# Optimization experiments

Measured on AMD Instinct MI355X. Metric: run time of the kernel, lower is better.

Reference implementation:

```python
import jax, jax.numpy as jnp
import numpy as np

G = 8       # groups
C = 64      # channels per group
KH = KW = 3 # kernel size
K = KH * KW
PAD = 1     # padding (stride=1, dilation=1)


def setup_inputs() -> dict:
    key = jax.random.key(0)
    k1, k2, k3 = jax.random.split(key, 3)
    B, H, W = 1, 100, 160
    x = jax.random.normal(k1, (B, H, W, G * C), dtype=jnp.float32)
    offset = jax.random.normal(k2, (B, H, W, G * K * 2), dtype=jnp.float32)
    mask = jax.random.normal(k3, (B, H, W, G * K), dtype=jnp.float32)
    return {"x": x, "offset": offset, "mask": mask}


def _dcn_core(x, offset, mask):
    B, H, W, _ = x.shape
    xg = x.reshape(B, H, W, G, C)
    off = offset.reshape(B, H, W, G, K, 2)
    m = jax.nn.softmax(mask.reshape(B, H, W, G, K), axis=-1)

    # kernel reference points relative to output pixel (stride=1, pad=1, dil=1)
    ky, kx = jnp.meshgrid(jnp.arange(KH, dtype=jnp.float32) - PAD,
                          jnp.arange(KW, dtype=jnp.float32) - PAD,
                          indexing="ij")
    ky = ky.reshape(K)  # [K]
    kx = kx.reshape(K)

    hh = jnp.arange(H, dtype=jnp.float32)[None, :, None, None, None]  # [1,H,1,1,1]
    ww = jnp.arange(W, dtype=jnp.float32)[None, None, :, None, None]  # [1,1,W,1,1]
    # sampling locations [B,H,W,G,K]
    loc_h = hh + ky[None, None, None, None, :] + off[..., 0]
    loc_w = ww + kx[None, None, None, None, :] + off[..., 1]

    h0 = jnp.floor(loc_h)
    w0 = jnp.floor(loc_w)
    th = loc_h - h0  # fractional parts
    tw = loc_w - w0
    h0 = h0.astype(jnp.int32)
    w0 = w0.astype(jnp.int32)

    b_idx = jnp.arange(B)[:, None, None, None, None]
    g_idx = jnp.arange(G)[None, None, None, :, None]

    def corner(hi, wi, wgt):
        valid = ((hi >= 0) & (hi < H) & (wi >= 0) & (wi < W)).astype(x.dtype)
        hi = jnp.clip(hi, 0, H - 1)
        wi = jnp.clip(wi, 0, W - 1)
        s = xg[b_idx, hi, wi, g_idx]            # [B,H,W,G,K,C]
        return s * (wgt * valid)[..., None]

    val = corner(h0,     w0,     (1 - th) * (1 - tw))
    val = val + corner(h0,     w0 + 1, (1 - th) * tw)
    val = val + corner(h0 + 1, w0,     th * (1 - tw))
    val = val + corner(h0 + 1, w0 + 1, th * tw)

    out = jnp.einsum("bhwgkc,bhwgk->bhwgc", val, m)  # modulated accumulate over K
    return out.reshape(B, H, W, G * C)


def reference(x, offset, mask):
    return _dcn_core(x, offset, mask)
```

## Files before the change

### kernel.cpp

```cpp
#include <hip/hip_runtime.h>
#include <hip/hip_fp16.h>

#define G_ 8
#define C_ 64
#define K_ 9
#define H_ 100
#define W_ 160
#define TW_ 8
#define TH_ 8
#define HALO_ 4
#define SW_ 16
#define SH_ 16
#define PLANE_ 273
#define TAB_ (8 * PLANE_)
#define NLDS_ (TAB_ + 576)

__global__ __launch_bounds__(512, 6) void dcn_kernel(
    const float* __restrict__ x,
    const float* __restrict__ offset,
    const float* __restrict__ mask,
    float* __restrict__ out)
{
    __shared__ uint4 sm[NLDS_];
    const int bid = (int)blockIdx.x;
    const int g   = bid & 7;
    const int t   = bid >> 3;
    const int th  = t / 20, twc = t % 20;
    const int h0  = th * TH_, w0 = twc * TW_;
    const int tid = (int)threadIdx.x;

#pragma unroll
    for (int it = 0; it < 4; ++it) {
        const int task = it * 512 + tid;
        const int rec  = task >> 3;
        const int c    = task & 7;
        const int i = rec >> 4, j = rec & 15;
        const int hs = min(max(h0 - HALO_ + i, 0), H_ - 1);
        const int ws = min(max(w0 - HALO_ + j, 0), W_ - 1);
        const float* src = x + (size_t)(hs * W_ + ws) * (G_ * C_) + g * C_ + c * 8;
        const float4 A = *(const float4*)src;
        const float4 B = *(const float4*)(src + 4);
        __half2 p0 = __floats2half2_rn(A.x, A.y);
        __half2 p1 = __floats2half2_rn(A.z, A.w);
        __half2 p2 = __floats2half2_rn(B.x, B.y);
        __half2 p3 = __floats2half2_rn(B.z, B.w);
        uint4 v;
        v.x = *(unsigned*)&p0; v.y = *(unsigned*)&p1;
        v.z = *(unsigned*)&p2; v.w = *(unsigned*)&p3;
        sm[c * PLANE_ + i * 17 + j] = v;
    }

    for (int task = tid; task < 576; task += 512) {
        const int px = task / 9;
        const int k  = task - px * 9;
        const int hh = h0 + (px >> 3), ww = w0 + (px & 7);
        uint4 r; r.x = 0u; r.y = 0u; r.z = 0u; r.w = 0u;
        if (hh < H_) {
            const int pixg = (hh * W_ + ww) * G_ + g;
            const float* mptr = mask + (size_t)pixg * K_;
            float mmax = -1e30f;
#pragma unroll
            for (int kk = 0; kk < K_; ++kk) mmax = fmaxf(mmax, mptr[kk]);
            float msum = 0.f;
#pragma unroll
            for (int kk = 0; kk < K_; ++kk) msum += __expf(mptr[kk] - mmax);
            const float m = __expf(mptr[k] - mmax) / msum;

            const float2 o2 = *(const float2*)(offset + (size_t)pixg * (2 * K_) + 2 * k);
            const float lh = (float)(hh + k / 3 - 1) + o2.x;
            const float lw = (float)(ww + k % 3 - 1) + o2.y;
            const float fh0 = floorf(lh), fw0 = floorf(lw);
            const float ft = lh - fh0, gt = lw - fw0;
            const int hI = (int)fh0, wI = (int)fw0;

            const float wh0 = (hI >= 0  && hI < H_    ) ? (1.f - ft) * m : 0.f;
            const float wh1 = (hI >= -1 && hI < H_ - 1) ? ft * m         : 0.f;
            const float cw0 = (wI >= 0  && wI < W_    ) ? (1.f - gt)     : 0.f;
            const float cw1 = (wI >= -1 && wI < W_ - 1) ? gt             : 0.f;
            __half2 wa = __floats2half2_rn(wh0 * cw0, wh0 * cw1);
            __half2 wb = __floats2half2_rn(wh1 * cw0, wh1 * cw1);

            const int hc0 = min(max(hI,     0), H_ - 1);
            const int hc1 = min(max(hI + 1, 0), H_ - 1);
            const int wc0 = min(max(wI,     0), W_ - 1);
            const int wc1 = min(max(wI + 1, 0), W_ - 1);

            const bool inbox = (hI >= h0 - HALO_) && (hI <= h0 + TH_ + HALO_ - 2) &&
                               (wI >= w0 - HALO_) && (wI <= w0 + TW_ + HALO_ - 2);
            if (inbox) {
                const int ri0 = hc0 - (h0 - HALO_);
                const int rj0 = wc0 - (w0 - HALO_);
                r.x = *(unsigned*)&wa;
                r.y = *(unsigned*)&wb;
                r.z = (unsigned)ri0 | ((unsigned)rj0 << 8)
                    | ((unsigned)(wc1 - wc0) << 16) | ((unsigned)(hc1 - hc0) << 17);
            } else {
                const int ri0 = min(max(hc0 - (h0 - HALO_), 0), SH_ - 1);
                const int rj0 = min(max(wc0 - (w0 - HALO_), 0), SW_ - 1);
                r.z = (unsigned)ri0 | ((unsigned)rj0 << 8) | 0x80000000u;
            }
        }
        sm[TAB_ + task] = r;
    }
    __syncthreads();

    const int px = tid >> 3;
    const int c  = tid & 7;
    const int hh = h0 + (px >> 3), ww = w0 + (px & 7);
    if (hh >= H_) return;
    const int pixg = (hh * W_ + ww) * G_ + g;
    const int pb = c * PLANE_;

    const uint4 t0 = sm[TAB_ + px * 9 + 0];
    const uint4 t1 = sm[TAB_ + px * 9 + 1];
    const uint4 t2 = sm[TAB_ + px * 9 + 2];
    const uint4 t3 = sm[TAB_ + px * 9 + 3];
    const uint4 t4 = sm[TAB_ + px * 9 + 4];
    const uint4 t5 = sm[TAB_ + px * 9 + 5];
    const uint4 t6 = sm[TAB_ + px * 9 + 6];
    const uint4 t7 = sm[TAB_ + px * 9 + 7];
    const uint4 t8 = sm[TAB_ + px * 9 + 8];

    __half2 acc[3][4];
#pragma unroll
    for (int gr = 0; gr < 3; ++gr)
#pragma unroll
        for (int u = 0; u < 4; ++u) acc[gr][u] = __half2(__half(0.f), __half(0.f));

#define FMA4(V, WD, GR)                                                       \
    {                                                                         \
        const __half2 wt_ = *(const __half2*)&(WD);                           \
        acc[GR][0] = __hfma2(*(const __half2*)&(V).x, wt_, acc[GR][0]);       \
        acc[GR][1] = __hfma2(*(const __half2*)&(V).y, wt_, acc[GR][1]);       \
        acc[GR][2] = __hfma2(*(const __half2*)&(V).z, wt_, acc[GR][2]);       \
        acc[GR][3] = __hfma2(*(const __half2*)&(V).w, wt_, acc[GR][3]);       \
    }

#define GC(GR, HC, WC, WF)                                                    \
    {                                                                         \
        const __half2 wt_ = __float2half2_rn(WF);                             \
        const float* s_ = x + (size_t)((HC) * W_ + (WC)) * (G_ * C_) + g * C_ + c * 8; \
        const float4 v0 = *(const float4*)s_;                                 \
        const float4 v1 = *(const float4*)(s_ + 4);                           \
        __half2 e0 = __floats2half2_rn(v0.x, v0.y), e1 = __floats2half2_rn(v0.z, v0.w); \
        __half2 e2 = __floats2half2_rn(v1.x, v1.y), e3 = __floats2half2_rn(v1.z, v1.w); \
        acc[GR][0] = __hfma2(e0, wt_, acc[GR][0]);                            \
        acc[GR][1] = __hfma2(e1, wt_, acc[GR][1]);                            \
        acc[GR][2] = __hfma2(e2, wt_, acc[GR][2]);                            \
        acc[GR][3] = __hfma2(e3, wt_, acc[GR][3]);                            \
    }

#define SLOWTAP(KK)                                                           \
    {                                                                         \
        const float* mptr_ = mask + (size_t)pixg * K_;                        \
        float mmax_ = -1e30f;                                                 \
        _Pragma("unroll")                                                     \
        for (int kk = 0; kk < K_; ++kk) mmax_ = fmaxf(mmax_, mptr_[kk]);      \
        float msum_ = 0.f;                                                    \
        _Pragma("unroll")                                                     \
        for (int kk = 0; kk < K_; ++kk) msum_ += __expf(mptr_[kk] - mmax_);   \
        const float m_ = __expf(mptr_[KK] - mmax_) / msum_;                   \
        const float2 o2_ = *(const float2*)(offset + (size_t)pixg * (2 * K_) + 2 * (KK)); \
        const float lh_ = (float)(hh + (KK) / 3 - 1) + o2_.x;                 \
        const float lw_ = (float)(ww + (KK) % 3 - 1) + o2_.y;                 \
        const float fh_ = floorf(lh_), fw_ = floorf(lw_);                     \
        const float ft_ = lh_ - fh_, gt_ = lw_ - fw_;                         \
        const int hI_ = (int)fh_, wI_ = (int)fw_;                             \
        const float wh0_ = (hI_ >= 0  && hI_ < H_    ) ? (1.f - ft_) * m_ : 0.f; \
        const float wh1_ = (hI_ >= -1 && hI_ < H_ - 1) ? ft_ * m_         : 0.f; \
        const float cw0_ = (wI_ >= 0  && wI_ < W_    ) ? (1.f - gt_)     : 0.f; \
        const float cw1_ = (wI_ >= -1 && wI_ < W_ - 1) ? gt_             : 0.f; \
        const int hc0_ = min(max(hI_,     0), H_ - 1);                        \
        const int hc1_ = min(max(hI_ + 1, 0), H_ - 1);                        \
        const int wc0_ = min(max(wI_,     0), W_ - 1);                        \
        const int wc1_ = min(max(wI_ + 1, 0), W_ - 1);                        \
        GC((KK) / 3, hc0_, wc0_, wh0_ * cw0_)                                 \
        GC((KK) / 3, hc0_, wc1_, wh0_ * cw1_)                                 \
        GC((KK) / 3, hc1_, wc0_, wh1_ * cw0_)                                 \
        GC((KK) / 3, hc1_, wc1_, wh1_ * cw1_)                                 \
    }

#define TAP(KK, R)                                                            \
    {                                                                         \
        const int ri0_ = (int)((R).z & 0xffu);                                \
        const int rj0_ = (int)(((R).z >> 8) & 0xffu);                         \
        const int dc_  = (int)(((R).z >> 16) & 1u);                           \
        const int dr17_ = (((R).z >> 17) & 1u) ? 17 : 0;                      \
        const int i00_ = pb + ri0_ * 17 + rj0_;                               \
        const int i01_ = i00_ + dc_;                                          \
        const int i10_ = i00_ + dr17_;                                        \
        const int i11_ = i10_ + dc_;                                          \
        const unsigned W00d = __builtin_amdgcn_perm((R).x, (R).x, 0x01000100u); \
        const unsigned W01d = __builtin_amdgcn_perm((R).x, (R).x, 0x03020302u); \
        const unsigned W10d = __builtin_amdgcn_perm((R).y, (R).y, 0x01000100u); \
        const unsigned W11d = __builtin_amdgcn_perm((R).y, (R).y, 0x03020302u); \
        const uint4 vA_ = sm[i00_];                                           \
        const uint4 vB_ = sm[i01_];                                           \
        const uint4 vC_ = sm[i10_];                                           \
        const uint4 vD_ = sm[i11_];                                           \
        FMA4(vA_, W00d, (KK) / 3)                                             \
        FMA4(vB_, W01d, (KK) / 3)                                             \
        FMA4(vC_, W10d, (KK) / 3)                                             \
        FMA4(vD_, W11d, (KK) / 3)                                             \
        if (__builtin_expect(((R).z >> 31) != 0u, 0)) { SLOWTAP(KK) }         \
    }

    TAP(0, t0) TAP(1, t1) TAP(2, t2)
    TAP(3, t3) TAP(4, t4) TAP(5, t5)
    TAP(6, t6) TAP(7, t7) TAP(8, t8)

#undef TAP
#undef SLOWTAP
#undef GC
#undef FMA4

    float* op = out + (size_t)pixg * C_ + c * 8;
    {
        const float2 s0 = __half22float2(acc[0][0]);
        const float2 a0 = __half22float2(acc[1][0]);
        const float2 b0 = __half22float2(acc[2][0]);
        const float2 s1 = __half22float2(acc[0][1]);
        const float2 a1 = __half22float2(acc[1][1]);
        const float2 b1 = __half22float2(acc[2][1]);
        const float2 s2 = __half22float2(acc[0][2]);
        const float2 a2 = __half22float2(acc[1][2]);
        const float2 b2 = __half22float2(acc[2][2]);
        const float2 s3 = __half22float2(acc[0][3]);
        const float2 a3 = __half22float2(acc[1][3]);
        const float2 b3 = __half22float2(acc[2][3]);
        float4 o1, o2;
        o1.x = s0.x + a0.x + b0.x;  o1.y = s0.y + a0.y + b0.y;
        o1.z = s1.x + a1.x + b1.x;  o1.w = s1.y + a1.y + b1.y;
        o2.x = s2.x + a2.x + b2.x;  o2.y = s2.y + a2.y + b2.y;
        o2.z = s3.x + a3.x + b3.x;  o2.w = s3.y + a3.y + b3.y;
        *(float4*)op       = o1;
        *(float4*)(op + 4) = o2;
    }
}

extern "C" void kernel_launch(void* const* d_in, const int* in_sizes, int n_in,
                              void* d_out, int out_size, void* d_ws, size_t ws_size,
                              hipStream_t stream) {
    const float* x      = (const float*)d_in[0];
    const float* offset = (const float*)d_in[1];
    const float* mask   = (const float*)d_in[2];
    float* out          = (float*)d_out;

    dcn_kernel<<<2080, 512, 0, stream>>>(x, offset, mask, out);
}
```

Measured before the change: 30.30 us.

## Swizzle LDS tile layout, split tap table into SoA arrays, raise occupancy

Replaces the padded-row (stride 17) LDS layout for the fp16 input halo with a 16-wide row layout using an XOR swizzle on the column index, shrinking LDS per plane. The per-tap table moves from a uint4 array, which carried an unused word, to three separate unsigned arrays loaded lazily inside each tap rather than all up front. Launch bounds rise from 6 to 8 blocks per CU to exploit the smaller LDS footprint and lower register pressure. The swizzle adds index arithmetic per corner and may change bank-conflict patterns for the gather reads.

```diff
diff --git a/kernel.cpp b/kernel.cpp
--- a/kernel.cpp
+++ b/kernel.cpp
@@ -11,17 +11,18 @@
 #define HALO_ 4
 #define SW_ 16
 #define SH_ 16
-#define PLANE_ 273
-#define TAB_ (8 * PLANE_)
-#define NLDS_ (TAB_ + 576)
-
-__global__ __launch_bounds__(512, 6) void dcn_kernel(
+#define PLANE_ 257
+#define NXP_ (8 * PLANE_)
+
+__global__ __launch_bounds__(512, 8) void dcn_kernel(
     const float* __restrict__ x,
     const float* __restrict__ offset,
     const float* __restrict__ mask,
     float* __restrict__ out)
 {
-    __shared__ uint4 sm[NLDS_];
+    __shared__ uint4 smx[NXP_];
+    __shared__ unsigned smw0[576], smw1[576], smidx[576];
+
     const int bid = (int)blockIdx.x;
     const int g   = bid & 7;
     const int t   = bid >> 3;
@@ -47,14 +48,14 @@
         uint4 v;
         v.x = *(unsigned*)&p0; v.y = *(unsigned*)&p1;
         v.z = *(unsigned*)&p2; v.w = *(unsigned*)&p3;
-        sm[c * PLANE_ + i * 17 + j] = v;
+        smx[c * PLANE_ + i * 16 + (j ^ (i & 7))] = v;
     }
 
     for (int task = tid; task < 576; task += 512) {
         const int px = task / 9;
         const int k  = task - px * 9;
         const int hh = h0 + (px >> 3), ww = w0 + (px & 7);
-        uint4 r; r.x = 0u; r.y = 0u; r.z = 0u; r.w = 0u;
+        unsigned rw0 = 0u, rw1 = 0u, ridx = 0u;
         if (hh < H_) {
             const int pixg = (hh * W_ + ww) * G_ + g;
             const float* mptr = mask + (size_t)pixg * K_;
@@ -90,17 +91,19 @@
             if (inbox) {
                 const int ri0 = hc0 - (h0 - HALO_);
                 const int rj0 = wc0 - (w0 - HALO_);
-                r.x = *(unsigned*)&wa;
-                r.y = *(unsigned*)&wb;
-                r.z = (unsigned)ri0 | ((unsigned)rj0 << 8)
-                    | ((unsigned)(wc1 - wc0) << 16) | ((unsigned)(hc1 - hc0) << 17);
+                rw0 = *(unsigned*)&wa;
+                rw1 = *(unsigned*)&wb;
+                ridx = (unsigned)ri0 | ((unsigned)rj0 << 8)
+                     | ((unsigned)(wc1 - wc0) << 16) | ((unsigned)(hc1 - hc0) << 17);
             } else {
                 const int ri0 = min(max(hc0 - (h0 - HALO_), 0), SH_ - 1);
                 const int rj0 = min(max(wc0 - (w0 - HALO_), 0), SW_ - 1);
-                r.z = (unsigned)ri0 | ((unsigned)rj0 << 8) | 0x80000000u;
+                ridx = (unsigned)ri0 | ((unsigned)rj0 << 8) | 0x80000000u;
             }
         }
-        sm[TAB_ + task] = r;
+        smw0[task] = rw0;
+        smw1[task] = rw1;
+        smidx[task] = ridx;
     }
     __syncthreads();
 
@@ -110,16 +113,7 @@
     if (hh >= H_) return;
     const int pixg = (hh * W_ + ww) * G_ + g;
     const int pb = c * PLANE_;
-
-    const uint4 t0 = sm[TAB_ + px * 9 + 0];
-    const uint4 t1 = sm[TAB_ + px * 9 + 1];
-    const uint4 t2 = sm[TAB_ + px * 9 + 2];
-    const uint4 t3 = sm[TAB_ + px * 9 + 3];
-    const uint4 t4 = sm[TAB_ + px * 9 + 4];
-    const uint4 t5 = sm[TAB_ + px * 9 + 5];
-    const uint4 t6 = sm[TAB_ + px * 9 + 6];
-    const uint4 t7 = sm[TAB_ + px * 9 + 7];
-    const uint4 t8 = sm[TAB_ + px * 9 + 8];
+    const int tb = px * 9;
 
     __half2 acc[3][4];
 #pragma unroll
@@ -180,34 +174,41 @@
         GC((KK) / 3, hc1_, wc1_, wh1_ * cw1_)                                 \
     }
 
-#define TAP(KK, R)                                                            \
-    {                                                                         \
-        const int ri0_ = (int)((R).z & 0xffu);                                \
-        const int rj0_ = (int)(((R).z >> 8) & 0xffu);                         \
-        const int dc_  = (int)(((R).z >> 16) & 1u);                           \
-        const int dr17_ = (((R).z >> 17) & 1u) ? 17 : 0;                      \
-        const int i00_ = pb + ri0_ * 17 + rj0_;                               \
-        const int i01_ = i00_ + dc_;                                          \
-        const int i10_ = i00_ + dr17_;                                        \
-        const int i11_ = i10_ + dc_;                                          \
-        const unsigned W00d = __builtin_amdgcn_perm((R).x, (R).x, 0x01000100u); \
-        const unsigned W01d = __builtin_amdgcn_perm((R).x, (R).x, 0x03020302u); \
-        const unsigned W10d = __builtin_amdgcn_perm((R).y, (R).y, 0x01000100u); \
-        const unsigned W11d = __builtin_amdgcn_perm((R).y, (R).y, 0x03020302u); \
-        const uint4 vA_ = sm[i00_];                                           \
-        const uint4 vB_ = sm[i01_];                                           \
-        const uint4 vC_ = sm[i10_];                                           \
-        const uint4 vD_ = sm[i11_];                                           \
+#define TAP(KK)                                                               \
+    {                                                                         \
+        const unsigned ridx_ = smidx[tb + (KK)];                              \
+        const unsigned rw0_  = smw0[tb + (KK)];                               \
+        const unsigned rw1_  = smw1[tb + (KK)];                               \
+        const int ri0_ = (int)(ridx_ & 0xffu);                                \
+        const int rj0_ = (int)((ridx_ >> 8) & 0xffu);                         \
+        const int dc_  = (int)((ridx_ >> 16) & 1u);                           \
+        const int dr_  = (int)((ridx_ >> 17) & 1u);                           \
+        const int ri1_ = ri0_ + dr_;                                          \
+        const int rj1_ = rj0_ + dc_;                                          \
+        const int s0_  = ri0_ & 7, s1_ = ri1_ & 7;                            \
+        const int row0_ = pb + ri0_ * 16, row1_ = pb + ri1_ * 16;             \
+        const int i00_ = row0_ + (rj0_ ^ s0_);                                \
+        const int i01_ = row0_ + (rj1_ ^ s0_);                                \
+        const int i10_ = row1_ + (rj0_ ^ s1_);                                \
+        const int i11_ = row1_ + (rj1_ ^ s1_);                                \
+        const unsigned W00d = __builtin_amdgcn_perm(rw0_, rw0_, 0x01000100u); \
+        const unsigned W01d = __builtin_amdgcn_perm(rw0_, rw0_, 0x03020302u); \
+        const unsigned W10d = __builtin_amdgcn_perm(rw1_, rw1_, 0x01000100u); \
+        const unsigned W11d = __builtin_amdgcn_perm(rw1_, rw1_, 0x03020302u); \
+        const uint4 vA_ = smx[i00_];                                          \
+        const uint4 vB_ = smx[i01_];                                          \
+        const uint4 vC_ = smx[i10_];                                          \
+        const uint4 vD_ = smx[i11_];                                          \
         FMA4(vA_, W00d, (KK) / 3)                                             \
         FMA4(vB_, W01d, (KK) / 3)                                             \
         FMA4(vC_, W10d, (KK) / 3)                                             \
         FMA4(vD_, W11d, (KK) / 3)                                             \
-        if (__builtin_expect(((R).z >> 31) != 0u, 0)) { SLOWTAP(KK) }         \
-    }
-
-    TAP(0, t0) TAP(1, t1) TAP(2, t2)
-    TAP(3, t3) TAP(4, t4) TAP(5, t5)
-    TAP(6, t6) TAP(7, t7) TAP(8, t8)
+        if (__builtin_expect((ridx_ >> 31) != 0u, 0)) { SLOWTAP(KK) }         \
+    }
+
+    TAP(0) TAP(1) TAP(2)
+    TAP(3) TAP(4) TAP(5)
+    TAP(6) TAP(7) TAP(8)
 
 #undef TAP
 #undef SLOWTAP
```

After: 29.81 us. No clear change (-1.6%).
